# Optimization experiments

Hardware: AMD Instinct MI355X
Metric: run time of the kernel (lower is better)

The kernel has to match this reference:

```python
import jax, jax.numpy as jnp
import numpy as np

TOP_K = 2
NUM_EXPERTS = 8
CAPACITY_FACTOR = 1.0


def setup_inputs() -> dict:
    key = jax.random.key(0)
    k1, k2, k3, k4 = jax.random.split(key, 4)
    sl, bs, hs, ffn = 2048, 2, 1024, 4096
    x = jax.random.normal(k1, (sl, bs, hs), dtype=jnp.float32)
    router_w = jax.random.normal(k2, (hs, NUM_EXPERTS), dtype=jnp.float32) * 0.02
    w1 = jax.random.normal(k3, (NUM_EXPERTS, hs, ffn), dtype=jnp.float32) * 0.02
    w2 = jax.random.normal(k4, (NUM_EXPERTS, ffn, hs), dtype=jnp.float32) * 0.02
    bias = jnp.zeros((1, 1, hs), dtype=jnp.float32)
    return {"x": x, "router_w": router_w, "w1": w1, "w2": w2, "bias": bias}


def _moe_forward(x, router_w, w1, w2):
    sl, bs, hs = x.shape
    xf = x.reshape(-1, hs)                                   # [T, H]
    T = xf.shape[0]
    TK = T * TOP_K
    capacity = int(CAPACITY_FACTOR * TOP_K * T / NUM_EXPERTS)  # static

    # Router: softmax over experts, then top-k (LearnedRouter)
    scores = jax.nn.softmax(xf @ router_w, axis=-1)          # [T, E]
    expert_weights, top_experts = jax.lax.top_k(scores, TOP_K)  # [T, K]
    ew = expert_weights.reshape(-1)                          # [T*K]
    te = top_experts.reshape(-1).astype(jnp.int32)           # [T*K]

    # indices_and_bins: stable sort by expert id + histogram + inclusive cumsum
    indices = jnp.argsort(te, stable=True)                   # sorted pos -> flat slot
    tokens_per_expert = jnp.zeros((NUM_EXPERTS,), jnp.int32).at[te].add(1)
    bins = jnp.cumsum(tokens_per_expert)                     # inclusive cumsum
    starts = bins - tokens_per_expert                        # exclusive offsets

    # binned_gather -> [E, capacity, H]; tokens beyond capacity are dropped
    c_range = jnp.arange(capacity)
    pos = starts[:, None] + c_range[None, :]                 # [E, C] positions in sorted order
    valid = c_range[None, :] < tokens_per_expert[:, None]    # [E, C]
    slot = indices[jnp.clip(pos, 0, TK - 1)]                 # flat (token*K + k) slot
    tok = slot // TOP_K                                      # source token row
    gathered = jnp.where(valid[..., None], xf[tok], 0.0)     # [E, C, H]

    # grouped expert MLP: gelu(x @ w1) @ w2  (megablocks mlp.MLP)
    h = jax.nn.gelu(jnp.einsum('ech,ehf->ecf', gathered, w1))
    y = jnp.einsum('ecf,efh->ech', h, w2)                    # [E, C, H]

    # binned_scatter: weighted accumulate back to token rows
    p = jnp.arange(TK)
    e_of_p = jnp.searchsorted(bins, p, side='right')         # expert of sorted pos
    c_of_p = p - starts[e_of_p]                              # slot within expert bin
    ok = c_of_p < capacity                                   # dropped tokens contribute 0
    vals = jnp.where(ok[:, None], y[e_of_p, jnp.clip(c_of_p, 0, capacity - 1)], 0.0)
    flat = indices                                           # flat slot at sorted pos p
    w = ew[flat]
    out = jnp.zeros((T, hs), x.dtype).at[flat // TOP_K].add(w[:, None] * vals)
    return out.reshape(sl, bs, hs)


def reference(x, router_w, w1, w2, bias):
    out = _moe_forward(x, router_w, w1, w2)
    return (out, bias)
```

## Files before the change

### kernel.cpp

```cpp
#include <hip/hip_runtime.h>
#include <hip/hip_bf16.h>


#define T_TOK 4096
#define HS 1024
#define FFN 4096
#define NE 8
#define CAP 1024
#define TKS 8192

#define WS_TE   67108864
#define WS_EW   67141632
#define WS_PERM 67174400
#define WS_WT   67239936
#define WS_XB   134348800

typedef float f4 __attribute__((ext_vector_type(4)));
typedef __bf16 bf16x8 __attribute__((ext_vector_type(8)));
typedef float f32x4 __attribute__((ext_vector_type(4)));

__device__ __forceinline__ void gld_lds16(const void* g, void* l) {
    __builtin_amdgcn_global_load_lds(
        (const __attribute__((address_space(1))) unsigned int*)g,
        (__attribute__((address_space(3))) unsigned int*)l, 16, 0, 0);
}

__global__ void init_out_kernel(float* __restrict__ out, const float* __restrict__ bias) {
    int i = blockIdx.x * 256 + threadIdx.x;
    const int TH = T_TOK * HS;
    if (i < TH) out[i] = 0.0f;
    else if (i < TH + HS) out[i] = bias[i - TH];
}

__global__ __launch_bounds__(256) void router_kernel(const float* __restrict__ x,
                                                     const float* __restrict__ rw,
                                                     int* __restrict__ te,
                                                     float* __restrict__ ew,
                                                     __bf16* __restrict__ xb) {
    __shared__ float rwt[NE * HS];
    int tid = threadIdx.x;
    for (int i = tid; i < NE * HS; i += 256) {
        int h = i >> 3, e = i & 7;
        rwt[e * HS + h] = rw[i];
    }
    __syncthreads();
    int wave = tid >> 6, lane = tid & 63;
    int t = blockIdx.x * 4 + wave;
    const float* xr = x + (size_t)t * HS;
    float s[NE];
    float xv[16];
#pragma unroll
    for (int e = 0; e < NE; ++e) s[e] = 0.0f;
#pragma unroll
    for (int j = 0; j < 16; ++j) {
        int h = lane + j * 64;
        xv[j] = xr[h];
#pragma unroll
        for (int e = 0; e < NE; ++e) s[e] += xv[j] * rwt[e * HS + h];
    }
#pragma unroll
    for (int j = 0; j < 16; ++j)
        xb[(size_t)t * HS + lane + j * 64] = (__bf16)xv[j];
#pragma unroll
    for (int e = 0; e < NE; ++e) {
#pragma unroll
        for (int off = 1; off < 64; off <<= 1) s[e] += __shfl_xor(s[e], off, 64);
    }
    float m = s[0];
#pragma unroll
    for (int e = 1; e < NE; ++e) m = fmaxf(m, s[e]);
    float psum = 0.0f;
#pragma unroll
    for (int e = 0; e < NE; ++e) psum += __expf(s[e] - m);
    int e0 = 0; float v0 = s[0];
#pragma unroll
    for (int e = 1; e < NE; ++e) { if (s[e] > v0) { v0 = s[e]; e0 = e; } }
    int e1 = -1; float v1 = -1e30f;
#pragma unroll
    for (int e = 0; e < NE; ++e) { if (e != e0 && s[e] > v1) { v1 = s[e]; e1 = e; } }
    if (lane == 0) {
        float inv = 1.0f / psum;
        te[2 * t]     = e0;
        te[2 * t + 1] = e1;
        ew[2 * t]     = __expf(v0 - m) * inv;
        ew[2 * t + 1] = __expf(v1 - m) * inv;
    }
}

__global__ __launch_bounds__(256) void sort_kernel(const int* __restrict__ te,
                                                   int* __restrict__ perm) {
    __shared__ int hist[256 * NE];
    int tid = threadIdx.x;
#pragma unroll
    for (int e = 0; e < NE; ++e) hist[tid * NE + e] = 0;
    for (int i = tid; i < TKS; i += 256) perm[i] = -1;
    __syncthreads();
    for (int j = 0; j < 32; ++j) {
        int p = tid * 32 + j;
        hist[tid * NE + te[p]]++;
    }
    __syncthreads();
    if (tid < NE) {
        int run = 0;
        for (int i = 0; i < 256; ++i) {
            int v = hist[i * NE + tid];
            hist[i * NE + tid] = run;
            run += v;
        }
    }
    __syncthreads();
    for (int j = 0; j < 32; ++j) {
        int p = tid * 32 + j;
        int e = te[p];
        int c = hist[tid * NE + e]++;
        if (c < CAP) perm[e * CAP + c] = p;
    }
}

__global__ __launch_bounds__(256) void conv_wt_kernel(const float* __restrict__ w,
                                                      __bf16* __restrict__ wt,
                                                      int K, int N) {
    __shared__ __bf16 t[64][72];
    const int e = blockIdx.z;
    const int kb = blockIdx.y * 64, nb = blockIdx.x * 64;
    const int tid = threadIdx.x;
    const float* src = w + ((size_t)e * K + kb) * N + nb;
    {
        const int kk = tid >> 4, nc = (tid & 15) * 4;
#pragma unroll
        for (int i = 0; i < 4; ++i) {
            int k = kk + 16 * i;
            f4 v = *(const f4*)(src + (size_t)k * N + nc);
            t[nc + 0][k] = (__bf16)v[0];
            t[nc + 1][k] = (__bf16)v[1];
            t[nc + 2][k] = (__bf16)v[2];
            t[nc + 3][k] = (__bf16)v[3];
        }
    }
    __syncthreads();
    __bf16* dst = wt + ((size_t)e * N + nb) * K + kb;
    const int nn = tid >> 3, ch = (tid & 7) * 8;
#pragma unroll
    for (int i = 0; i < 2; ++i) {
        int n = nn + 32 * i;
        bf16x8 v = *(const bf16x8*)(&t[n][ch]);
        *(bf16x8*)(dst + (size_t)n * K + ch) = v;
    }
}


#define STAGE8(koff_) do {                                                  \
    _Pragma("unroll")                                                       \
    for (int j = 0; j < 4; ++j) {                                           \
        gld_lds16(aptr[j] + (koff_), &As[j * 32 + w * 8][0]);               \
        gld_lds16(bptr[j] + (koff_), &Bs[j * 32 + w * 8][0]);               \
    }                                                                       \
} while (0)

#define TILE_BODY() do {                                                    \
    _Pragma("unroll")                                                       \
    for (int kk = 0; kk < 2; ++kk) {                                        \
        const int g = (kk * 4 + (lane >> 4)) ^ (lane & 7);                  \
        bf16x8 af[4], bb[4];                                                \
        _Pragma("unroll")                                                   \
        for (int mi = 0; mi < 4; ++mi)                                      \
            af[mi] = *(const bf16x8*)&As[wr * 64 + mi * 16 + l15][g * 8];   \
        _Pragma("unroll")                                                   \
        for (int ni = 0; ni < 4; ++ni)                                      \
            bb[ni] = *(const bf16x8*)&Bs[wc * 64 + ni * 16 + l15][g * 8];   \
        __builtin_amdgcn_s_setprio(1);                                      \
        _Pragma("unroll")                                                   \
        for (int mi = 0; mi < 4; ++mi)                                      \
            _Pragma("unroll")                                               \
            for (int ni = 0; ni < 4; ++ni)                                  \
                acc[mi][ni] = __builtin_amdgcn_mfma_f32_16x16x32_bf16(      \
                    af[mi], bb[ni], acc[mi][ni], 0, 0, 0);                  \
        __builtin_amdgcn_s_setprio(0);                                      \
    }                                                                       \
} while (0)

#define KLOOP(NT_) do {                                                     \
    for (int t = 0; t < (NT_); ++t) {                                       \
        STAGE8(t * 64);                                                     \
        asm volatile("s_waitcnt vmcnt(0)" ::: "memory");                    \
        __syncthreads();                                                    \
        TILE_BODY();                                                        \
        __syncthreads();                                                    \
    }                                                                       \
} while (0)

__global__ __launch_bounds__(256) void gemm1_kernel(const __bf16* __restrict__ xb,
                                                    const __bf16* __restrict__ w1t,
                                                    const int* __restrict__ perm,
                                                    __bf16* __restrict__ hbuf) {
    __shared__ __bf16 As[128][64];
    __shared__ __bf16 Bs[128][64];
    const int hw = blockIdx.x;
    const int logical = (hw & 7) * 256 + (hw >> 3);
    const int nblk = logical & 31;
    const int mblk = (logical >> 5) & 7;
    const int e    = logical >> 8;
    const int tid = threadIdx.x, lane = tid & 63, w = tid >> 6;
    const int wr = w >> 1, wc = w & 1;
    const int l15 = lane & 15;
    const int srl = lane >> 3;
    const int gsrc = (lane & 7) ^ srl;

    const __bf16* aptr[4];
    const __bf16* bptr[4];
#pragma unroll
    for (int j = 0; j < 4; ++j) {
        int arow = j * 32 + w * 8 + srl;
        int p = perm[e * CAP + mblk * 128 + arow];
        int tok = (p < 0) ? 0 : (p >> 1);
        aptr[j] = xb + (size_t)tok * HS + gsrc * 8;
        int brow = nblk * 128 + j * 32 + w * 8 + srl;
        bptr[j] = w1t + ((size_t)e * FFN + brow) * HS + gsrc * 8;
    }

    f32x4 acc[4][4];
#pragma unroll
    for (int mi = 0; mi < 4; ++mi)
#pragma unroll
        for (int ni = 0; ni < 4; ++ni) acc[mi][ni] = (f32x4)0.0f;

    KLOOP(HS / 64);

    const int mbase = mblk * 128 + wr * 64;
    const int nbase = nblk * 128 + wc * 64;
#pragma unroll
    for (int mi = 0; mi < 4; ++mi) {
#pragma unroll
        for (int ni = 0; ni < 4; ++ni) {
#pragma unroll
            for (int reg = 0; reg < 4; ++reg) {
                int mrow = mbase + mi * 16 + (lane >> 4) * 4 + reg;
                int ncol = nbase + ni * 16 + l15;
                float z = acc[mi][ni][reg];
                float z2 = z * z;
                float y = z * (1.5957691216057308f + 0.07135481627f * z2);
                float ex = __expf(-y);
                float gv = z * __builtin_amdgcn_rcpf(1.0f + ex);
                hbuf[(size_t)(e * CAP + mrow) * FFN + ncol] = (__bf16)gv;
            }
        }
    }
}

__global__ __launch_bounds__(256) void gemm2_kernel(const __bf16* __restrict__ hbuf,
                                                    const __bf16* __restrict__ w2t,
                                                    const int* __restrict__ perm,
                                                    const float* __restrict__ ew,
                                                    float* __restrict__ out) {
    __shared__ __bf16 As[128][64];
    __shared__ __bf16 Bs[128][64];
    const int hw = blockIdx.x;
    const int logical = (hw & 7) * 64 + (hw >> 3);
    const int nblk = logical & 7;
    const int mblk = (logical >> 3) & 7;
    const int e    = logical >> 6;
    const int tid = threadIdx.x, lane = tid & 63, w = tid >> 6;
    const int wr = w >> 1, wc = w & 1;
    const int l15 = lane & 15;
    const int srl = lane >> 3;
    const int gsrc = (lane & 7) ^ srl;

    const __bf16* aptr[4];
    const __bf16* bptr[4];
#pragma unroll
    for (int j = 0; j < 4; ++j) {
        int arow = j * 32 + w * 8 + srl;
        aptr[j] = hbuf + ((size_t)(e * CAP + mblk * 128 + arow)) * FFN + gsrc * 8;
        int brow = nblk * 128 + j * 32 + w * 8 + srl;
        bptr[j] = w2t + ((size_t)e * HS + brow) * FFN + gsrc * 8;
    }

    f32x4 acc[4][4];
#pragma unroll
    for (int mi = 0; mi < 4; ++mi)
#pragma unroll
        for (int ni = 0; ni < 4; ++ni) acc[mi][ni] = (f32x4)0.0f;

    KLOOP(FFN / 64);

    int* sperm = (int*)&As[0][0];
    float* swt = (float*)(sperm + 128);
    if (tid < 128) {
        int p = perm[e * CAP + mblk * 128 + tid];
        sperm[tid] = p;
        swt[tid] = (p >= 0) ? ew[p] : 0.0f;
    }
    __syncthreads();

    const int nbase = nblk * 128 + wc * 64;
#pragma unroll
    for (int mi = 0; mi < 4; ++mi) {
#pragma unroll
        for (int reg = 0; reg < 4; ++reg) {
            int mloc = wr * 64 + mi * 16 + (lane >> 4) * 4 + reg;
            int p = sperm[mloc];
            if (p >= 0) {
                int tok = p >> 1;
                float wgt = swt[mloc];
#pragma unroll
                for (int ni = 0; ni < 4; ++ni) {
                    int n = nbase + ni * 16 + l15;
                    atomicAdd(&out[(size_t)tok * HS + n], wgt * acc[mi][ni][reg]);
                }
            }
        }
    }
}

extern "C" void kernel_launch(void* const* d_in, const int* in_sizes, int n_in,
                              void* d_out, int out_size, void* d_ws, size_t ws_size,
                              hipStream_t stream) {
    const float* x    = (const float*)d_in[0];
    const float* rw   = (const float*)d_in[1];
    const float* w1   = (const float*)d_in[2];
    const float* w2   = (const float*)d_in[3];
    const float* bias = (const float*)d_in[4];
    float* out = (float*)d_out;
    char* ws = (char*)d_ws;

    __bf16* hbuf = (__bf16*)ws;
    int*    te   = (int*)(ws + WS_TE);
    float*  ew   = (float*)(ws + WS_EW);
    int*    perm = (int*)(ws + WS_PERM);
    __bf16* wt   = (__bf16*)(ws + WS_WT);
    __bf16* xb   = (__bf16*)(ws + WS_XB);

    hipLaunchKernelGGL(init_out_kernel, dim3((T_TOK * HS + HS + 255) / 256), dim3(256),
                       0, stream, out, bias);
    hipLaunchKernelGGL(router_kernel, dim3(T_TOK / 4), dim3(256), 0, stream,
                       x, rw, te, ew, xb);
    hipLaunchKernelGGL(sort_kernel, dim3(1), dim3(256), 0, stream, te, perm);
    hipLaunchKernelGGL(conv_wt_kernel, dim3(FFN / 64, HS / 64, NE), dim3(256),
                       0, stream, w1, wt, HS, FFN);
    hipLaunchKernelGGL(gemm1_kernel, dim3(2048), dim3(256), 0, stream,
                       xb, wt, perm, hbuf);
    hipLaunchKernelGGL(conv_wt_kernel, dim3(HS / 64, FFN / 64, NE), dim3(256),
                       0, stream, w2, wt, FFN, HS);
    hipLaunchKernelGGL(gemm2_kernel, dim3(512), dim3(256), 0, stream,
                       hbuf, wt, perm, ew, out);
}
```

Baseline: 281.4 us.

## Fuse pre-processing kernels, overlap w2 conversion with gemm1, split-K gemm2

Merges the router, w1 bf16 transpose and output initialisation into one kernel. It appends the w2 transpose as extra blocks of gemm1 when the workspace is large enough, so conversion overlaps GEMM work. It also splits gemm2's K dimension in two to double block count. The aim is to cut launch overhead and serial conversion time and to raise gemm2 occupancy, at the cost of more atomic accumulation and a larger workspace.

```diff
diff --git a/kernel.cpp b/kernel.cpp
--- a/kernel.cpp
+++ b/kernel.cpp
@@ -14,6 +14,8 @@
 #define WS_PERM 67174400
 #define WS_WT   67239936
 #define WS_XB   134348800
+#define WS_W2T  142737408
+#define WS_W2T_END (WS_W2T + 67108864)
 
 typedef float f4 __attribute__((ext_vector_type(4)));
 typedef __bf16 bf16x8 __attribute__((ext_vector_type(8)));
@@ -25,65 +27,102 @@
         (__attribute__((address_space(3))) unsigned int*)l, 16, 0, 0);
 }
 
-__global__ void init_out_kernel(float* __restrict__ out, const float* __restrict__ bias) {
-    int i = blockIdx.x * 256 + threadIdx.x;
-    const int TH = T_TOK * HS;
-    if (i < TH) out[i] = 0.0f;
-    else if (i < TH + HS) out[i] = bias[i - TH];
-}
-
-__global__ __launch_bounds__(256) void router_kernel(const float* __restrict__ x,
-                                                     const float* __restrict__ rw,
-                                                     int* __restrict__ te,
-                                                     float* __restrict__ ew,
-                                                     __bf16* __restrict__ xb) {
+__global__ __launch_bounds__(256) void fused_pre_kernel(const float* __restrict__ x,
+                                                        const float* __restrict__ rw,
+                                                        int* __restrict__ te,
+                                                        float* __restrict__ ew,
+                                                        __bf16* __restrict__ xb,
+                                                        const float* __restrict__ w1,
+                                                        __bf16* __restrict__ w1t,
+                                                        float* __restrict__ out,
+                                                        const float* __restrict__ bias) {
     __shared__ float rwt[NE * HS];
-    int tid = threadIdx.x;
-    for (int i = tid; i < NE * HS; i += 256) {
-        int h = i >> 3, e = i & 7;
-        rwt[e * HS + h] = rw[i];
-    }
-    __syncthreads();
-    int wave = tid >> 6, lane = tid & 63;
-    int t = blockIdx.x * 4 + wave;
-    const float* xr = x + (size_t)t * HS;
-    float s[NE];
-    float xv[16];
-#pragma unroll
-    for (int e = 0; e < NE; ++e) s[e] = 0.0f;
-#pragma unroll
-    for (int j = 0; j < 16; ++j) {
-        int h = lane + j * 64;
-        xv[j] = xr[h];
-#pragma unroll
-        for (int e = 0; e < NE; ++e) s[e] += xv[j] * rwt[e * HS + h];
-    }
-#pragma unroll
-    for (int j = 0; j < 16; ++j)
-        xb[(size_t)t * HS + lane + j * 64] = (__bf16)xv[j];
-#pragma unroll
-    for (int e = 0; e < NE; ++e) {
-#pragma unroll
-        for (int off = 1; off < 64; off <<= 1) s[e] += __shfl_xor(s[e], off, 64);
-    }
-    float m = s[0];
-#pragma unroll
-    for (int e = 1; e < NE; ++e) m = fmaxf(m, s[e]);
-    float psum = 0.0f;
-#pragma unroll
-    for (int e = 0; e < NE; ++e) psum += __expf(s[e] - m);
-    int e0 = 0; float v0 = s[0];
-#pragma unroll
-    for (int e = 1; e < NE; ++e) { if (s[e] > v0) { v0 = s[e]; e0 = e; } }
-    int e1 = -1; float v1 = -1e30f;
-#pragma unroll
-    for (int e = 0; e < NE; ++e) { if (e != e0 && s[e] > v1) { v1 = s[e]; e1 = e; } }
-    if (lane == 0) {
-        float inv = 1.0f / psum;
-        te[2 * t]     = e0;
-        te[2 * t + 1] = e1;
-        ew[2 * t]     = __expf(v0 - m) * inv;
-        ew[2 * t + 1] = __expf(v1 - m) * inv;
+    const int b = blockIdx.x;
+    const int tid = threadIdx.x;
+
+    if (b < 1024) {
+        for (int i = tid; i < NE * HS; i += 256) {
+            int h = i >> 3, e = i & 7;
+            rwt[e * HS + h] = rw[i];
+        }
+        __syncthreads();
+        int wave = tid >> 6, lane = tid & 63;
+        int t = b * 4 + wave;
+        const float* xr = x + (size_t)t * HS;
+        float s[NE];
+        float xv[16];
+#pragma unroll
+        for (int e = 0; e < NE; ++e) s[e] = 0.0f;
+#pragma unroll
+        for (int j = 0; j < 16; ++j) {
+            int h = lane + j * 64;
+            xv[j] = xr[h];
+#pragma unroll
+            for (int e = 0; e < NE; ++e) s[e] += xv[j] * rwt[e * HS + h];
+        }
+#pragma unroll
+        for (int j = 0; j < 16; ++j)
+            xb[(size_t)t * HS + lane + j * 64] = (__bf16)xv[j];
+#pragma unroll
+        for (int e = 0; e < NE; ++e) {
+#pragma unroll
+            for (int off = 1; off < 64; off <<= 1) s[e] += __shfl_xor(s[e], off, 64);
+        }
+        float m = s[0];
+#pragma unroll
+        for (int e = 1; e < NE; ++e) m = fmaxf(m, s[e]);
+        float psum = 0.0f;
+#pragma unroll
+        for (int e = 0; e < NE; ++e) psum += __expf(s[e] - m);
+        int e0 = 0; float v0 = s[0];
+#pragma unroll
+        for (int e = 1; e < NE; ++e) { if (s[e] > v0) { v0 = s[e]; e0 = e; } }
+        int e1 = -1; float v1 = -1e30f;
+#pragma unroll
+        for (int e = 0; e < NE; ++e) { if (e != e0 && s[e] > v1) { v1 = s[e]; e1 = e; } }
+        if (lane == 0) {
+            float inv = 1.0f / psum;
+            te[2 * t]     = e0;
+            te[2 * t + 1] = e1;
+            ew[2 * t]     = __expf(v0 - m) * inv;
+            ew[2 * t + 1] = __expf(v1 - m) * inv;
+        }
+    } else if (b < 9216) {
+        __bf16 (*t)[72] = (__bf16(*)[72])rwt;
+        const int cb = b - 1024;
+        const int e = cb >> 10, r = cb & 1023;
+        const int kb = (r >> 6) * 64, nb = (r & 63) * 64;
+        const float* src = w1 + ((size_t)e * HS + kb) * FFN + nb;
+        {
+            const int kk = tid >> 4, nc = (tid & 15) * 4;
+#pragma unroll
+            for (int i = 0; i < 4; ++i) {
+                int k = kk + 16 * i;
+                f4 v = *(const f4*)(src + (size_t)k * FFN + nc);
+                t[nc + 0][k] = (__bf16)v[0];
+                t[nc + 1][k] = (__bf16)v[1];
+                t[nc + 2][k] = (__bf16)v[2];
+                t[nc + 3][k] = (__bf16)v[3];
+            }
+        }
+        __syncthreads();
+        __bf16* dst = w1t + ((size_t)e * FFN + nb) * HS + kb;
+        const int nn = tid >> 3, ch = (tid & 7) * 8;
+#pragma unroll
+        for (int i = 0; i < 2; ++i) {
+            int n = nn + 32 * i;
+            bf16x8 v = *(const bf16x8*)(&t[n][ch]);
+            *(bf16x8*)(dst + (size_t)n * HS + ch) = v;
+        }
+    } else {
+        const int TOT4 = (T_TOK * HS + HS) >> 2;
+        const int TH4  = (T_TOK * HS) >> 2;
+        const int idx = (b - 9216) * 256 + tid;
+        for (int i4 = idx; i4 < TOT4; i4 += 2048 * 256) {
+            f4 v = (f4)0.0f;
+            if (i4 >= TH4) v = *(const f4*)(bias + (((size_t)i4 - TH4) << 2));
+            *(f4*)(out + ((size_t)i4 << 2)) = v;
+        }
     }
 }
 
@@ -192,15 +231,52 @@
 __global__ __launch_bounds__(256) void gemm1_kernel(const __bf16* __restrict__ xb,
                                                     const __bf16* __restrict__ w1t,
                                                     const int* __restrict__ perm,
-                                                    __bf16* __restrict__ hbuf) {
+                                                    __bf16* __restrict__ hbuf,
+                                                    const float* __restrict__ w2,
+                                                    __bf16* __restrict__ w2t,
+                                                    int fused) {
     __shared__ __bf16 As[128][64];
     __shared__ __bf16 Bs[128][64];
+    const int tid = threadIdx.x;
+
+    if (blockIdx.x >= 2048) {
+        if (fused) {
+            __bf16 (*t)[72] = (__bf16(*)[72])(&As[0][0]);
+            const int cb = blockIdx.x - 2048;
+            const int e = cb >> 10, r = cb & 1023;
+            const int kb = (r >> 4) * 64, nb = (r & 15) * 64;
+            const float* src = w2 + ((size_t)e * FFN + kb) * HS + nb;
+            {
+                const int kk = tid >> 4, nc = (tid & 15) * 4;
+#pragma unroll
+                for (int i = 0; i < 4; ++i) {
+                    int k = kk + 16 * i;
+                    f4 v = *(const f4*)(src + (size_t)k * HS + nc);
+                    t[nc + 0][k] = (__bf16)v[0];
+                    t[nc + 1][k] = (__bf16)v[1];
+                    t[nc + 2][k] = (__bf16)v[2];
+                    t[nc + 3][k] = (__bf16)v[3];
+                }
+            }
+            __syncthreads();
+            __bf16* dst = w2t + ((size_t)e * HS + nb) * FFN + kb;
+            const int nn = tid >> 3, ch = (tid & 7) * 8;
+#pragma unroll
+            for (int i = 0; i < 2; ++i) {
+                int n = nn + 32 * i;
+                bf16x8 v = *(const bf16x8*)(&t[n][ch]);
+                *(bf16x8*)(dst + (size_t)n * FFN + ch) = v;
+            }
+        }
+        return;
+    }
+
     const int hw = blockIdx.x;
     const int logical = (hw & 7) * 256 + (hw >> 3);
     const int nblk = logical & 31;
     const int mblk = (logical >> 5) & 7;
     const int e    = logical >> 8;
-    const int tid = threadIdx.x, lane = tid & 63, w = tid >> 6;
+    const int lane = tid & 63, w = tid >> 6;
     const int wr = w >> 1, wc = w & 1;
     const int l15 = lane & 15;
     const int srl = lane >> 3;
@@ -255,24 +331,28 @@
     __shared__ __bf16 As[128][64];
     __shared__ __bf16 Bs[128][64];
     const int hw = blockIdx.x;
-    const int logical = (hw & 7) * 64 + (hw >> 3);
-    const int nblk = logical & 7;
-    const int mblk = (logical >> 3) & 7;
-    const int e    = logical >> 6;
+    const int logical = (hw & 7) * 128 + (hw >> 3);
+    const int e    = logical >> 7;
+    const int idx  = logical & 127;
+    const int half = idx >> 6;
+    const int mblk = (idx >> 3) & 7;
+    const int nblk = idx & 7;
     const int tid = threadIdx.x, lane = tid & 63, w = tid >> 6;
     const int wr = w >> 1, wc = w & 1;
     const int l15 = lane & 15;
     const int srl = lane >> 3;
     const int gsrc = (lane & 7) ^ srl;
+    const size_t kbase = (size_t)half * 2048;
 
     const __bf16* aptr[4];
     const __bf16* bptr[4];
 #pragma unroll
     for (int j = 0; j < 4; ++j) {
         int arow = j * 32 + w * 8 + srl;
-        aptr[j] = hbuf + ((size_t)(e * CAP + mblk * 128 + arow)) * FFN + gsrc * 8;
+        aptr[j] = hbuf + ((size_t)(e * CAP + mblk * 128 + arow)) * FFN
+                  + kbase + gsrc * 8;
         int brow = nblk * 128 + j * 32 + w * 8 + srl;
-        bptr[j] = w2t + ((size_t)e * HS + brow) * FFN + gsrc * 8;
+        bptr[j] = w2t + ((size_t)e * HS + brow) * FFN + kbase + gsrc * 8;
     }
 
     f32x4 acc[4][4];
@@ -281,7 +361,7 @@
 #pragma unroll
         for (int ni = 0; ni < 4; ++ni) acc[mi][ni] = (f32x4)0.0f;
 
-    KLOOP(FFN / 64);
+    KLOOP(2048 / 64);
 
     int* sperm = (int*)&As[0][0];
     float* swt = (float*)(sperm + 128);
@@ -329,18 +409,19 @@
     int*    perm = (int*)(ws + WS_PERM);
     __bf16* wt   = (__bf16*)(ws + WS_WT);
     __bf16* xb   = (__bf16*)(ws + WS_XB);
-
-    hipLaunchKernelGGL(init_out_kernel, dim3((T_TOK * HS + HS + 255) / 256), dim3(256),
-                       0, stream, out, bias);
-    hipLaunchKernelGGL(router_kernel, dim3(T_TOK / 4), dim3(256), 0, stream,
-                       x, rw, te, ew, xb);
+    __bf16* w2t  = (__bf16*)(ws + WS_W2T);
+
+    const int fused = (ws_size >= (size_t)WS_W2T_END) ? 1 : 0;
+    __bf16* w2dst = fused ? w2t : wt;
+
+    hipLaunchKernelGGL(fused_pre_kernel, dim3(11264), dim3(256), 0, stream,
+                       x, rw, te, ew, xb, w1, wt, out, bias);
     hipLaunchKernelGGL(sort_kernel, dim3(1), dim3(256), 0, stream, te, perm);
-    hipLaunchKernelGGL(conv_wt_kernel, dim3(FFN / 64, HS / 64, NE), dim3(256),
-                       0, stream, w1, wt, HS, FFN);
-    hipLaunchKernelGGL(gemm1_kernel, dim3(2048), dim3(256), 0, stream,
-                       xb, wt, perm, hbuf);
-    hipLaunchKernelGGL(conv_wt_kernel, dim3(HS / 64, FFN / 64, NE), dim3(256),
-                       0, stream, w2, wt, FFN, HS);
-    hipLaunchKernelGGL(gemm2_kernel, dim3(512), dim3(256), 0, stream,
-                       hbuf, wt, perm, ew, out);
-}
+    hipLaunchKernelGGL(gemm1_kernel, dim3(fused ? 10240 : 2048), dim3(256), 0, stream,
+                       xb, wt, perm, hbuf, w2, w2t, fused);
+    if (!fused)
+        hipLaunchKernelGGL(conv_wt_kernel, dim3(HS / 64, FFN / 64, NE), dim3(256),
+                           0, stream, w2, wt, FFN, HS);
+    hipLaunchKernelGGL(gemm2_kernel, dim3(1024), dim3(256), 0, stream,
+                       hbuf, w2dst, perm, ew, out);
+}
```

After: 310.2 us. 1.1x slower.

## Enlarge gemm1 tile to 256x256 with 8 waves and interleaved LDS reads

Applied to the files above, without the earlier changes.

gemm1 moves from 128x128 tiles with 4 waves to 256x256 tiles with 8 waves per 512-thread block, and the grid becomes 3D with 512 blocks. The K-step body is split into staged LDS reads via inline ds_read_b128, with explicit lgkmcnt waits and sched barriers interleaved with MFMA groups. The aim is more data reuse per global load and overlap of LDS reads with MFMAs. In exchange it uses more registers and LDS per block and launches fewer blocks, which may reduce occupancy. gemm2 keeps the old 128x128 loop.

```diff
diff --git a/kernel.cpp b/kernel.cpp
--- a/kernel.cpp
+++ b/kernel.cpp
@@ -23,6 +23,13 @@
     __builtin_amdgcn_global_load_lds(
         (const __attribute__((address_space(1))) unsigned int*)g,
         (__attribute__((address_space(3))) unsigned int*)l, 16, 0, 0);
+}
+
+__device__ __forceinline__ bf16x8 ds_read16(const void* p) {
+    bf16x8 r;
+    unsigned off = (unsigned)(size_t)(const __attribute__((address_space(3))) char*)p;
+    asm volatile("ds_read_b128 %0, %1" : "=&v"(r) : "v"(off));
+    return r;
 }
 
 __global__ void init_out_kernel(float* __restrict__ out, const float* __restrict__ bias) {
@@ -149,59 +156,82 @@
 }
 
 
-#define STAGE8(koff_) do {                                                  \
+#define LGKM0() do {                                                        \
+    asm volatile("s_waitcnt lgkmcnt(0)" ::: "memory");                      \
+    __builtin_amdgcn_sched_barrier(0);                                      \
+} while (0)
+
+#define STAGE_A1(h_, koff_) do {                                            \
+    gld_lds16(aptr[(h_)*2 + 0] + (koff_), &As[(h_)*128 + w*16 + 0][0]);     \
+    gld_lds16(aptr[(h_)*2 + 1] + (koff_), &As[(h_)*128 + w*16 + 8][0]);     \
+} while (0)
+
+#define STAGE_B1(h_, koff_) do {                                            \
+    gld_lds16(bptr[(h_)*2 + 0] + (koff_), &Bs[(h_)*128 + w*16 + 0][0]);     \
+    gld_lds16(bptr[(h_)*2 + 1] + (koff_), &Bs[(h_)*128 + w*16 + 8][0]);     \
+} while (0)
+
+#define RD_A4(MB_) do {                                                     \
     _Pragma("unroll")                                                       \
-    for (int j = 0; j < 4; ++j) {                                           \
-        gld_lds16(aptr[j] + (koff_), &As[j * 32 + w * 8][0]);               \
-        gld_lds16(bptr[j] + (koff_), &Bs[j * 32 + w * 8][0]);               \
-    }                                                                       \
-} while (0)
-
-#define TILE_BODY() do {                                                    \
+    for (int mi = 0; mi < 4; ++mi)                                          \
+        _Pragma("unroll")                                                   \
+        for (int kk = 0; kk < 2; ++kk)                                      \
+            a[mi][kk] = ds_read16(&As[wr*128 + ((MB_)+mi)*16 + l15]         \
+                            [(((kk*4 + (lane>>4)) ^ (lane&7)) * 8)]);       \
+} while (0)
+
+#define RD_B2(NB_) do {                                                     \
     _Pragma("unroll")                                                       \
-    for (int kk = 0; kk < 2; ++kk) {                                        \
-        const int g = (kk * 4 + (lane >> 4)) ^ (lane & 7);                  \
-        bf16x8 af[4], bb[4];                                                \
-        _Pragma("unroll")                                                   \
-        for (int mi = 0; mi < 4; ++mi)                                      \
-            af[mi] = *(const bf16x8*)&As[wr * 64 + mi * 16 + l15][g * 8];   \
-        _Pragma("unroll")                                                   \
-        for (int ni = 0; ni < 4; ++ni)                                      \
-            bb[ni] = *(const bf16x8*)&Bs[wc * 64 + ni * 16 + l15][g * 8];   \
-        __builtin_amdgcn_s_setprio(1);                                      \
-        _Pragma("unroll")                                                   \
-        for (int mi = 0; mi < 4; ++mi)                                      \
+    for (int ni = 0; ni < 2; ++ni)                                          \
+        _Pragma("unroll")                                                   \
+        for (int kk = 0; kk < 2; ++kk)                                      \
+            b[(NB_)+ni][kk] = ds_read16(&Bs[wc*64 + ((NB_)+ni)*16 + l15]    \
+                            [(((kk*4 + (lane>>4)) ^ (lane&7)) * 8)]);       \
+} while (0)
+
+#define MFMA16(MB_, NB_) do {                                               \
+    __builtin_amdgcn_s_setprio(1);                                          \
+    _Pragma("unroll")                                                       \
+    for (int mi = 0; mi < 4; ++mi)                                          \
+        _Pragma("unroll")                                                   \
+        for (int ni = 0; ni < 2; ++ni)                                      \
             _Pragma("unroll")                                               \
-            for (int ni = 0; ni < 4; ++ni)                                  \
-                acc[mi][ni] = __builtin_amdgcn_mfma_f32_16x16x32_bf16(      \
-                    af[mi], bb[ni], acc[mi][ni], 0, 0, 0);                  \
-        __builtin_amdgcn_s_setprio(0);                                      \
-    }                                                                       \
-} while (0)
-
-#define KLOOP(NT_) do {                                                     \
+            for (int kk = 0; kk < 2; ++kk)                                  \
+                acc[(MB_)+mi][(NB_)+ni] = __builtin_amdgcn_mfma_f32_16x16x32_bf16(\
+                    a[mi][kk], b[(NB_)+ni][kk], acc[(MB_)+mi][(NB_)+ni], 0, 0, 0);\
+    __builtin_amdgcn_s_setprio(0);                                          \
+} while (0)
+
+#define KLOOP256(NT_) do {                                                  \
     for (int t = 0; t < (NT_); ++t) {                                       \
-        STAGE8(t * 64);                                                     \
+        STAGE_A1(0, t * 64); STAGE_A1(1, t * 64);                           \
+        STAGE_B1(0, t * 64); STAGE_B1(1, t * 64);                           \
         asm volatile("s_waitcnt vmcnt(0)" ::: "memory");                    \
         __syncthreads();                                                    \
-        TILE_BODY();                                                        \
+        RD_A4(0); RD_B2(0); LGKM0();                                        \
+        MFMA16(0, 0);                                                       \
+        RD_B2(2); LGKM0();                                                  \
+        MFMA16(0, 2);                                                       \
+        RD_A4(4); LGKM0();                                                  \
+        MFMA16(4, 2);                                                       \
+        MFMA16(4, 0);                                                       \
         __syncthreads();                                                    \
     }                                                                       \
 } while (0)
 
-__global__ __launch_bounds__(256) void gemm1_kernel(const __bf16* __restrict__ xb,
-                                                    const __bf16* __restrict__ w1t,
-                                                    const int* __restrict__ perm,
-                                                    __bf16* __restrict__ hbuf) {
-    __shared__ __bf16 As[128][64];
-    __shared__ __bf16 Bs[128][64];
-    const int hw = blockIdx.x;
-    const int logical = (hw & 7) * 256 + (hw >> 3);
-    const int nblk = logical & 31;
-    const int mblk = (logical >> 5) & 7;
-    const int e    = logical >> 8;
+__global__ __launch_bounds__(512, 4) void gemm1_kernel(const __bf16* __restrict__ xb,
+                                                       const __bf16* __restrict__ w1t,
+                                                       const int* __restrict__ perm,
+                                                       __bf16* __restrict__ hbuf) {
+    __shared__ __bf16 As[256][64];
+    __shared__ __bf16 Bs[256][64];
+    const int hw = blockIdx.x + 16 * blockIdx.y + 64 * blockIdx.z;
+    const int logical = (hw & 7) * 64 + (hw >> 3);
+    const int nblk = logical & 15;
+    const int mblk = (logical >> 4) & 3;
+    const int e    = logical >> 6;
     const int tid = threadIdx.x, lane = tid & 63, w = tid >> 6;
-    const int wr = w >> 1, wc = w & 1;
+    const int wr = w >> 2, wc = w & 3;
     const int l15 = lane & 15;
     const int srl = lane >> 3;
     const int gsrc = (lane & 7) ^ srl;
@@ -209,27 +239,31 @@
     const __bf16* aptr[4];
     const __bf16* bptr[4];
 #pragma unroll
-    for (int j = 0; j < 4; ++j) {
-        int arow = j * 32 + w * 8 + srl;
-        int p = perm[e * CAP + mblk * 128 + arow];
-        int tok = (p < 0) ? 0 : (p >> 1);
-        aptr[j] = xb + (size_t)tok * HS + gsrc * 8;
-        int brow = nblk * 128 + j * 32 + w * 8 + srl;
-        bptr[j] = w1t + ((size_t)e * FFN + brow) * HS + gsrc * 8;
-    }
-
-    f32x4 acc[4][4];
-#pragma unroll
-    for (int mi = 0; mi < 4; ++mi)
+    for (int h = 0; h < 2; ++h) {
+#pragma unroll
+        for (int o2 = 0; o2 < 2; ++o2) {
+            int r = h * 128 + w * 16 + o2 * 8 + srl;
+            int p = perm[e * CAP + mblk * 256 + r];
+            int tok = (p < 0) ? 0 : (p >> 1);
+            aptr[h * 2 + o2] = xb + (size_t)tok * HS + gsrc * 8;
+            int brow = nblk * 256 + r;
+            bptr[h * 2 + o2] = w1t + ((size_t)e * FFN + brow) * HS + gsrc * 8;
+        }
+    }
+
+    f32x4 acc[8][4];
+#pragma unroll
+    for (int mi = 0; mi < 8; ++mi)
 #pragma unroll
         for (int ni = 0; ni < 4; ++ni) acc[mi][ni] = (f32x4)0.0f;
-
-    KLOOP(HS / 64);
-
-    const int mbase = mblk * 128 + wr * 64;
-    const int nbase = nblk * 128 + wc * 64;
-#pragma unroll
-    for (int mi = 0; mi < 4; ++mi) {
+    bf16x8 a[4][2], b[4][2];
+
+    KLOOP256(HS / 64);
+
+    const int mbase = mblk * 256 + wr * 128;
+    const int nbase = nblk * 256 + wc * 64;
+#pragma unroll
+    for (int mi = 0; mi < 8; ++mi) {
 #pragma unroll
         for (int ni = 0; ni < 4; ++ni) {
 #pragma unroll
@@ -246,6 +280,47 @@
         }
     }
 }
+
+
+#define STAGE8(koff_) do {                                                  \
+    _Pragma("unroll")                                                       \
+    for (int j = 0; j < 4; ++j) {                                           \
+        gld_lds16(aptr[j] + (koff_), &As[j * 32 + w * 8][0]);               \
+        gld_lds16(bptr[j] + (koff_), &Bs[j * 32 + w * 8][0]);               \
+    }                                                                       \
+} while (0)
+
+#define TILE_BODY() do {                                                    \
+    _Pragma("unroll")                                                       \
+    for (int kk = 0; kk < 2; ++kk) {                                        \
+        const int g = (kk * 4 + (lane >> 4)) ^ (lane & 7);                  \
+        bf16x8 af[4], bb[4];                                                \
+        _Pragma("unroll")                                                   \
+        for (int mi = 0; mi < 4; ++mi)                                      \
+            af[mi] = *(const bf16x8*)&As[wr * 64 + mi * 16 + l15][g * 8];   \
+        _Pragma("unroll")                                                   \
+        for (int ni = 0; ni < 4; ++ni)                                      \
+            bb[ni] = *(const bf16x8*)&Bs[wc * 64 + ni * 16 + l15][g * 8];   \
+        __builtin_amdgcn_s_setprio(1);                                      \
+        _Pragma("unroll")                                                   \
+        for (int mi = 0; mi < 4; ++mi)                                      \
+            _Pragma("unroll")                                               \
+            for (int ni = 0; ni < 4; ++ni)                                  \
+                acc[mi][ni] = __builtin_amdgcn_mfma_f32_16x16x32_bf16(      \
+                    af[mi], bb[ni], acc[mi][ni], 0, 0, 0);                  \
+        __builtin_amdgcn_s_setprio(0);                                      \
+    }                                                                       \
+} while (0)
+
+#define KLOOP128(NT_) do {                                                  \
+    for (int t = 0; t < (NT_); ++t) {                                       \
+        STAGE8(t * 64);                                                     \
+        asm volatile("s_waitcnt vmcnt(0)" ::: "memory");                    \
+        __syncthreads();                                                    \
+        TILE_BODY();                                                        \
+        __syncthreads();                                                    \
+    }                                                                       \
+} while (0)
 
 __global__ __launch_bounds__(256) void gemm2_kernel(const __bf16* __restrict__ hbuf,
                                                     const __bf16* __restrict__ w2t,
@@ -281,7 +356,7 @@
 #pragma unroll
         for (int ni = 0; ni < 4; ++ni) acc[mi][ni] = (f32x4)0.0f;
 
-    KLOOP(FFN / 64);
+    KLOOP128(FFN / 64);
 
     int* sperm = (int*)&As[0][0];
     float* swt = (float*)(sperm + 128);
@@ -337,8 +412,8 @@
     hipLaunchKernelGGL(sort_kernel, dim3(1), dim3(256), 0, stream, te, perm);
     hipLaunchKernelGGL(conv_wt_kernel, dim3(FFN / 64, HS / 64, NE), dim3(256),
                        0, stream, w1, wt, HS, FFN);
-    hipLaunchKernelGGL(gemm1_kernel, dim3(2048), dim3(256), 0, stream,
-                       xb, wt, perm, hbuf);
+    hipLaunchKernelGGL(gemm1_kernel, dim3(FFN / 256, CAP / 256, NE), dim3(512),
+                       0, stream, xb, wt, perm, hbuf);
     hipLaunchKernelGGL(conv_wt_kernel, dim3(HS / 64, FFN / 64, NE), dim3(256),
                        0, stream, w2, wt, FFN, HS);
     hipLaunchKernelGGL(gemm2_kernel, dim3(512), dim3(256), 0, stream,
```

After: 702.1 us. 150% more time.
